# Kernel tuning notes

Hardware: AMD Instinct MI355X
Metric: run time of the kernel (lower is better)

## Reference

```python
import jax, jax.numpy as jnp
import numpy as np

B, S, D = 4, 4096, 64

def setup_inputs() -> dict:
    key = jax.random.key(0)
    kq, kk, kv, km = jax.random.split(key, 4)
    q = jax.random.normal(kq, (B, S, D), dtype=jnp.float32)
    k = jax.random.normal(kk, (B, S, D), dtype=jnp.float32)
    v = jax.random.normal(kv, (B, S, D), dtype=jnp.float32)
    # binary keep-mask in {0,1}; log(mask) -> {0, -inf}
    mask = (jax.random.uniform(km, (B, S)) > 0.2).astype(jnp.float32)
    return {"q": q, "k": k, "v": v, "mask": mask}

def reference(q, k, v, mask):
    emb_dim = q.shape[-1]
    qs = q / jnp.asarray(emb_dim, q.dtype) ** 0.5           # [B,S,D] scaled query
    scores = jnp.einsum('bqd,bkd->bqk', qs, k)              # [B,S,S]
    scores = scores + jnp.log(mask)[:, None, :]             # mask keys via log-add
    w = jax.nn.softmax(scores, axis=-1)                     # [B,S,S]
    out = jnp.einsum('bqk,bkd->bqd', w, v)                  # [B,S,D]
    # post-blend: masked query positions pass through the (scaled) query
    return out * mask[..., None] + qs * (1.0 - mask)[..., None]
```

## Files before the change

kernel.cpp:

```cpp
#include <hip/hip_runtime.h>
#include <hip/hip_bf16.h>

#define BATCH 4
#define SEQ   4096
#define DIM   64
#define TK    32

#if __has_builtin(__builtin_amdgcn_mfma_f32_16x16x16bf16_1k)
#define HAVE_1K 1
#else
#define HAVE_1K 0
#endif

typedef __attribute__((ext_vector_type(8))) short bf16x8;
typedef __attribute__((ext_vector_type(4))) short bf16x4;
typedef __attribute__((ext_vector_type(4))) float f32x4;

#define AS1 __attribute__((address_space(1)))
#define AS3 __attribute__((address_space(3)))

static __device__ __forceinline__ short f2bf(float x) {
    __hip_bfloat16 h = __float2bfloat16(x);
    return *reinterpret_cast<short*>(&h);
}
static __device__ __forceinline__ int pk2bf(float lo, float hi) {
    __hip_bfloat162 t = __float22bfloat162_rn(make_float2(lo, hi));
    int r; __builtin_memcpy(&r, &t, 4); return r;
}
static __device__ __forceinline__ bf16x4 mk4(const f32x4& s) {
    int2 t = make_int2(pk2bf(s[0], s[1]), pk2bf(s[2], s[3]));
    bf16x4 r; __builtin_memcpy(&r, &t, 8); return r;
}
static __device__ __forceinline__ void async16(const short* g, short* l) {
    __builtin_amdgcn_global_load_lds((const AS1 unsigned int*)g,
                                     (AS3 unsigned int*)l, 16, 0, 0);
}

__global__ __launch_bounds__(256)
void pack_kv(const float* __restrict__ kg, const float* __restrict__ vg,
             const float* __restrict__ mg,
             short* __restrict__ kp, short* __restrict__ vtp)
{
    if (blockIdx.x < 1024) {
        const int t   = blockIdx.x * 256 + threadIdx.x;
        const int row = t >> 4;
        const int d0  = (t & 15) * 4;
        f32x4 kv = *reinterpret_cast<const f32x4*>(kg + (size_t)row * DIM + d0);
        short4 ks;
        ks.x = f2bf(kv[0]); ks.y = f2bf(kv[1]); ks.z = f2bf(kv[2]); ks.w = f2bf(kv[3]);
        const int gs = (d0 >> 3) ^ (row & 7);
        *reinterpret_cast<short4*>(kp + (size_t)row * DIM + gs * 8 + (d0 & 7)) = ks;
    } else {
        __shared__ float Vl[64][66];
        __shared__ float Ml[64];
        const int t64 = blockIdx.x - 1024;
        const float* src = vg + (size_t)t64 * 64 * DIM;
        const int tid = threadIdx.x;
        #pragma unroll
        for (int i = 0; i < 4; ++i) {
            int idx = i * 256 + tid;
            int key = idx >> 4, part = idx & 15;
            f32x4 vv = *reinterpret_cast<const f32x4*>(src + (size_t)key * DIM + part * 4);
            float2* p0 = reinterpret_cast<float2*>(&Vl[key][part * 4]);
            p0[0] = make_float2(vv[0], vv[1]);
            p0[1] = make_float2(vv[2], vv[3]);
        }
        if (tid < 64) Ml[tid] = mg[(size_t)t64 * 64 + tid];
        __syncthreads();
        #pragma unroll
        for (int i = 0; i < 2; ++i) {
            const int gid = i * 256 + tid;
            const int t2 = gid >> 8;
            const int d  = (gid >> 2) & 63;
            const int g  = gid & 3;
            alignas(16) short s8[8];
            #pragma unroll
            for (int j = 0; j < 8; ++j) {
#if HAVE_1K
                const int key = t2 * 32 + (j >> 2) * 16 + g * 4 + (j & 3);
#else
                const int key = t2 * 32 + g * 8 + j;
#endif
                s8[j] = f2bf(Vl[key][d] * Ml[key]);
            }
            const int gs = g ^ ((d >> 1) & 3);
            short* dst = vtp + ((size_t)t64 * 2 + t2) * (TK * DIM) + d * TK + gs * 8;
            *reinterpret_cast<int4*>(dst) = *reinterpret_cast<const int4*>(s8);
        }
    }
}

template<int NSEG>
__global__ __launch_bounds__(256, 4)
void attn_fwd5(const float* __restrict__ qg, const float* __restrict__ mg,
               const short* __restrict__ kp, const short* __restrict__ vtp,
               float* __restrict__ outg, float* __restrict__ part)
{
    constexpr int SEGLEN = SEQ / NSEG;
    constexpr int ITERS  = SEGLEN / TK;

    __shared__ __align__(16) short Kl[2][TK][DIM];
    __shared__ __align__(16) short Vt[2][DIM][TK];

    const int tid  = threadIdx.x;
    const int wave = tid >> 6;
    const int lane = tid & 63;
    const int ln   = lane & 15;
    const int quad = lane >> 4;

    const int qblk = blockIdx.x & 31;
    const int rest = blockIdx.x >> 5;
    const int seg  = (NSEG == 1) ? 0 : (rest & (NSEG - 1));
    const int b    = (NSEG == 1) ? rest : (rest / NSEG);

    const int qw = qblk * 128 + wave * 32;
    const size_t bbase = (size_t)b * SEQ * DIM;

    const short* kb  = kp  + bbase + (size_t)seg * SEGLEN * DIM;
    const short* vb  = vtp + bbase + (size_t)seg * SEGLEN * DIM;
    const float* mgb = mg + (size_t)b * SEQ;

    const int gs0 = quad ^ (ln & 7);
    const int gsv = quad ^ ((ln >> 1) & 3);

#if !HAVE_1K
    const int idxA = ((lane & 16) * 2 + (lane & 15)) * 4;
    const int idxB = idxA + 64;
    const bool loquad = (quad < 2);
#endif

    bf16x8 aq[2][2];
    #pragma unroll
    for (int qt = 0; qt < 2; ++qt) {
        const float* qrow = qg + bbase + (size_t)(qw + qt * 16 + ln) * DIM;
        #pragma unroll
        for (int h = 0; h < 2; ++h) {
            alignas(16) short tmp[8];
            #pragma unroll
            for (int j = 0; j < 8; ++j)
                tmp[j] = f2bf(qrow[quad * 8 + h * 32 + j] * 0.125f);
            aq[qt][h] = *reinterpret_cast<bf16x8*>(tmp);
        }
    }

    f32x4 O[2][4];
    float lacc[2] = {0.f, 0.f};
    #pragma unroll
    for (int qt = 0; qt < 2; ++qt)
        #pragma unroll
        for (int i = 0; i < 4; ++i) O[qt][i] = (f32x4){0.f, 0.f, 0.f, 0.f};

    async16(kb + wave * 512 + lane * 8, &Kl[0][0][0] + wave * 512);
    async16(vb + wave * 512 + lane * 8, &Vt[0][0][0] + wave * 512);

    for (int t = 0; t < ITERS; ++t) {
        const int buf = t & 1;
        asm volatile("s_waitcnt vmcnt(0)" ::: "memory");
        __syncthreads();

        if (t + 1 < ITERS) {
            const short* gk = kb + (size_t)(t + 1) * TK * DIM;
            const short* gv = vb + (size_t)(t + 1) * TK * DIM;
            async16(gk + wave * 512 + lane * 8, &Kl[buf ^ 1][0][0] + wave * 512);
            async16(gv + wave * 512 + lane * 8, &Vt[buf ^ 1][0][0] + wave * 512);
        }

        const int key0 = seg * SEGLEN + t * TK;
        f32x4 m4[2];
        #pragma unroll
        for (int s = 0; s < 2; ++s)
            m4[s] = *reinterpret_cast<const f32x4*>(mgb + key0 + s * 16 + quad * 4);

        const short* klb = &Kl[buf][0][0];
        f32x4 sf[2][2];
        #pragma unroll
        for (int s = 0; s < 2; ++s) {
            bf16x8 ka0 = *reinterpret_cast<const bf16x8*>(klb + (s * 16 + ln) * DIM + gs0 * 8);
            bf16x8 ka1 = *reinterpret_cast<const bf16x8*>(klb + (s * 16 + ln) * DIM + (gs0 ^ 4) * 8);
            #pragma unroll
            for (int qt = 0; qt < 2; ++qt) {
                f32x4 acc = (f32x4){0.f, 0.f, 0.f, 0.f};
                acc = __builtin_amdgcn_mfma_f32_16x16x32_bf16(ka0, aq[qt][0], acc, 0, 0, 0);
                acc = __builtin_amdgcn_mfma_f32_16x16x32_bf16(ka1, aq[qt][1], acc, 0, 0, 0);
                sf[qt][s] = acc;
            }
        }

        #pragma unroll
        for (int qt = 0; qt < 2; ++qt)
            #pragma unroll
            for (int s = 0; s < 2; ++s)
                #pragma unroll
                for (int r = 0; r < 4; ++r) {
                    sf[qt][s][r] = __expf(sf[qt][s][r]);
                    lacc[qt] = fmaf(sf[qt][s][r], m4[s][r], lacc[qt]);
                }

        const short* vtb = &Vt[buf][0][0];
#if HAVE_1K
        bf16x4 bp[2][2];
        #pragma unroll
        for (int qt = 0; qt < 2; ++qt)
            #pragma unroll
            for (int s = 0; s < 2; ++s)
                bp[qt][s] = mk4(sf[qt][s]);
        #pragma unroll
        for (int ds = 0; ds < 4; ++ds) {
            bf16x8 vf = *reinterpret_cast<const bf16x8*>(vtb + (ds * 16 + ln) * TK + gsv * 8);
            bf16x4 va0 = __builtin_shufflevector(vf, vf, 0, 1, 2, 3);
            bf16x4 va1 = __builtin_shufflevector(vf, vf, 4, 5, 6, 7);
            #pragma unroll
            for (int qt = 0; qt < 2; ++qt) {
                O[qt][ds] = __builtin_amdgcn_mfma_f32_16x16x16bf16_1k(va0, bp[qt][0], O[qt][ds], 0, 0, 0);
                O[qt][ds] = __builtin_amdgcn_mfma_f32_16x16x16bf16_1k(va1, bp[qt][1], O[qt][ds], 0, 0, 0);
            }
        }
#else
        bf16x8 bfr[2];
        #pragma unroll
        for (int qt = 0; qt < 2; ++qt) {
            const int pk0_0 = pk2bf(sf[qt][0][0], sf[qt][0][1]);
            const int pk0_1 = pk2bf(sf[qt][0][2], sf[qt][0][3]);
            const int pk1_0 = pk2bf(sf[qt][1][0], sf[qt][1][1]);
            const int pk1_1 = pk2bf(sf[qt][1][2], sf[qt][1][3]);
            const int w0l = __builtin_amdgcn_ds_bpermute(idxA, pk0_0);
            const int w0h = __builtin_amdgcn_ds_bpermute(idxA, pk1_0);
            const int w1l = __builtin_amdgcn_ds_bpermute(idxA, pk0_1);
            const int w1h = __builtin_amdgcn_ds_bpermute(idxA, pk1_1);
            const int w2l = __builtin_amdgcn_ds_bpermute(idxB, pk0_0);
            const int w2h = __builtin_amdgcn_ds_bpermute(idxB, pk1_0);
            const int w3l = __builtin_amdgcn_ds_bpermute(idxB, pk0_1);
            const int w3h = __builtin_amdgcn_ds_bpermute(idxB, pk1_1);
            alignas(16) int bw[4];
            bw[0] = loquad ? w0l : w0h;
            bw[1] = loquad ? w1l : w1h;
            bw[2] = loquad ? w2l : w2h;
            bw[3] = loquad ? w3l : w3h;
            bfr[qt] = *reinterpret_cast<bf16x8*>(bw);
        }
        #pragma unroll
        for (int ds = 0; ds < 4; ++ds) {
            bf16x8 va = *reinterpret_cast<const bf16x8*>(vtb + (ds * 16 + ln) * TK + gsv * 8);
            #pragma unroll
            for (int qt = 0; qt < 2; ++qt)
                O[qt][ds] = __builtin_amdgcn_mfma_f32_16x16x32_bf16(va, bfr[qt], O[qt][ds], 0, 0, 0);
        }
#endif
    }

    #pragma unroll
    for (int qt = 0; qt < 2; ++qt) {
        lacc[qt] += __shfl_xor(lacc[qt], 16);
        lacc[qt] += __shfl_xor(lacc[qt], 32);
    }

    if (NSEG == 1) {
        #pragma unroll
        for (int qt = 0; qt < 2; ++qt) {
            const int qrow_i = qw + qt * 16 + ln;
            const float qm = mgb[qrow_i];
            const float inv = 1.0f / lacc[qt];
            const float* qrow = qg + bbase + (size_t)qrow_i * DIM;
            float* orow = outg + bbase + (size_t)qrow_i * DIM;
            #pragma unroll
            for (int ds = 0; ds < 4; ++ds) {
                const int d0 = ds * 16 + quad * 4;
                f32x4 o4;
                #pragma unroll
                for (int r = 0; r < 4; ++r) o4[r] = O[qt][ds][r] * inv;
                if (qm == 0.0f) {
                    f32x4 q4 = *reinterpret_cast<const f32x4*>(qrow + d0);
                    #pragma unroll
                    for (int r = 0; r < 4; ++r) o4[r] = q4[r] * 0.125f;
                }
                *reinterpret_cast<f32x4*>(orow + d0) = o4;
            }
        }
    } else {
        #pragma unroll
        for (int qt = 0; qt < 2; ++qt) {
            float* pb = part + (size_t)((b * SEQ + qw + qt * 16 + ln) * NSEG + seg) * 68;
            #pragma unroll
            for (int ds = 0; ds < 4; ++ds)
                *reinterpret_cast<f32x4*>(pb + ds * 16 + quad * 4) = O[qt][ds];
            if (quad == 0) pb[64] = lacc[qt];
        }
    }
}

template<int NSEG>
__global__ __launch_bounds__(256)
void combine_p(const float* __restrict__ part, const float* __restrict__ qg,
               const float* __restrict__ mg, float* __restrict__ outg)
{
    const int t = blockIdx.x * 256 + threadIdx.x;
    const int q = t >> 6;
    const int d = t & 63;
    const float* pb = part + (size_t)q * NSEG * 68;
    float acc = 0.f, den = 0.f;
    #pragma unroll
    for (int s = 0; s < NSEG; ++s) {
        acc += pb[s * 68 + d];
        den += pb[s * 68 + 64];
    }
    float out = acc / den;
    if (mg[q] == 0.0f) out = qg[t] * 0.125f;
    outg[t] = out;
}

extern "C" void kernel_launch(void* const* d_in, const int* in_sizes, int n_in,
                              void* d_out, int out_size, void* d_ws, size_t ws_size,
                              hipStream_t stream) {
    (void)in_sizes; (void)n_in; (void)out_size;
    const float* q = (const float*)d_in[0];
    const float* k = (const float*)d_in[1];
    const float* v = (const float*)d_in[2];
    const float* m = (const float*)d_in[3];
    float* out = (float*)d_out;

    const size_t nelem  = (size_t)BATCH * SEQ * DIM;
    const size_t packsz = nelem * 2 * sizeof(short);
    const size_t part8  = (size_t)BATCH * SEQ * 8 * 68 * sizeof(float);
    const size_t part4  = (size_t)BATCH * SEQ * 4 * 68 * sizeof(float);

    short* kp  = (short*)d_ws;
    short* vtp = kp + nelem;
    float* part = (float*)((char*)d_ws + packsz);

    pack_kv<<<dim3(1280), dim3(256), 0, stream>>>(k, v, m, kp, vtp);

    if (ws_size >= packsz + part8) {
        attn_fwd5<8><<<dim3(BATCH * 32 * 8), dim3(256), 0, stream>>>(q, m, kp, vtp, out, part);
        combine_p<8><<<dim3(BATCH * SEQ * DIM / 256), dim3(256), 0, stream>>>(part, q, m, out);
    } else if (ws_size >= packsz + part4) {
        attn_fwd5<4><<<dim3(BATCH * 32 * 4), dim3(256), 0, stream>>>(q, m, kp, vtp, out, part);
        combine_p<4><<<dim3(BATCH * SEQ * DIM / 256), dim3(256), 0, stream>>>(part, q, m, out);
    } else {
        attn_fwd5<1><<<dim3(BATCH * 32), dim3(256), 0, stream>>>(q, m, kp, vtp, out, nullptr);
    }
}
```

Baseline: 111.6 us.

## Double key tile to 64, use exp2 with folded log2e, repack V layout

```diff
diff --git a/kernel.cpp b/kernel.cpp
--- a/kernel.cpp
+++ b/kernel.cpp
@@ -4,7 +4,8 @@
 #define BATCH 4
 #define SEQ   4096
 #define DIM   64
-#define TK    32
+#define TK    64
+#define LOG2E 1.4426950408889634f
 
 #if __has_builtin(__builtin_amdgcn_mfma_f32_16x16x16bf16_1k)
 #define HAVE_1K 1
@@ -12,6 +13,12 @@
 #define HAVE_1K 0
 #endif
 
+#if __has_builtin(__builtin_amdgcn_exp2f)
+#define EXP2(x) __builtin_amdgcn_exp2f(x)
+#else
+#define EXP2(x) exp2f(x)
+#endif
+
 typedef __attribute__((ext_vector_type(8))) short bf16x8;
 typedef __attribute__((ext_vector_type(4))) short bf16x4;
 typedef __attribute__((ext_vector_type(4))) float f32x4;
@@ -30,6 +37,14 @@
 static __device__ __forceinline__ bf16x4 mk4(const f32x4& s) {
     int2 t = make_int2(pk2bf(s[0], s[1]), pk2bf(s[2], s[3]));
     bf16x4 r; __builtin_memcpy(&r, &t, 8); return r;
+}
+static __device__ __forceinline__ f32x4 mfma16(bf16x4 a, bf16x4 b, f32x4 c) {
+#if HAVE_1K
+    return __builtin_amdgcn_mfma_f32_16x16x16bf16_1k(a, b, c, 0, 0, 0);
+#else
+    asm("v_mfma_f32_16x16x16_bf16 %0, %1, %2, %0" : "+v"(c) : "v"(a), "v"(b));
+    return c;
+#endif
 }
 static __device__ __forceinline__ void async16(const short* g, short* l) {
     __builtin_amdgcn_global_load_lds((const AS1 unsigned int*)g,
@@ -41,20 +56,23 @@
              const float* __restrict__ mg,
              short* __restrict__ kp, short* __restrict__ vtp)
 {
-    if (blockIdx.x < 1024) {
-        const int t   = blockIdx.x * 256 + threadIdx.x;
-        const int row = t >> 4;
-        const int d0  = (t & 15) * 4;
-        f32x4 kv = *reinterpret_cast<const f32x4*>(kg + (size_t)row * DIM + d0);
-        short4 ks;
-        ks.x = f2bf(kv[0]); ks.y = f2bf(kv[1]); ks.z = f2bf(kv[2]); ks.w = f2bf(kv[3]);
-        const int gs = (d0 >> 3) ^ (row & 7);
-        *reinterpret_cast<short4*>(kp + (size_t)row * DIM + gs * 8 + (d0 & 7)) = ks;
+    if (blockIdx.x < 256) {
+        #pragma unroll
+        for (int i = 0; i < 4; ++i) {
+            const int unit = blockIdx.x * 1024 + i * 256 + threadIdx.x;
+            const int row = unit >> 4;
+            const int d0  = (unit & 15) * 4;
+            f32x4 kv = *reinterpret_cast<const f32x4*>(kg + (size_t)row * DIM + d0);
+            short4 ks;
+            ks.x = f2bf(kv[0]); ks.y = f2bf(kv[1]); ks.z = f2bf(kv[2]); ks.w = f2bf(kv[3]);
+            const int gs = (d0 >> 3) ^ (row & 7);
+            *reinterpret_cast<short4*>(kp + (size_t)row * DIM + gs * 8 + (d0 & 7)) = ks;
+        }
     } else {
         __shared__ float Vl[64][66];
         __shared__ float Ml[64];
-        const int t64 = blockIdx.x - 1024;
-        const float* src = vg + (size_t)t64 * 64 * DIM;
+        const int tile = blockIdx.x - 256;
+        const float* src = vg + (size_t)tile * TK * DIM;
         const int tid = threadIdx.x;
         #pragma unroll
         for (int i = 0; i < 4; ++i) {
@@ -65,26 +83,23 @@
             p0[0] = make_float2(vv[0], vv[1]);
             p0[1] = make_float2(vv[2], vv[3]);
         }
-        if (tid < 64) Ml[tid] = mg[(size_t)t64 * 64 + tid];
+        if (tid < 64) Ml[tid] = mg[(size_t)tile * TK + tid];
         __syncthreads();
         #pragma unroll
         for (int i = 0; i < 2; ++i) {
             const int gid = i * 256 + tid;
-            const int t2 = gid >> 8;
-            const int d  = (gid >> 2) & 63;
-            const int g  = gid & 3;
+            const int d = gid >> 3;
+            const int G = gid & 7;
+            const int qd = G >> 1, u = G & 1;
             alignas(16) short s8[8];
             #pragma unroll
-            for (int j = 0; j < 8; ++j) {
-#if HAVE_1K
-                const int key = t2 * 32 + (j >> 2) * 16 + g * 4 + (j & 3);
-#else
-                const int key = t2 * 32 + g * 8 + j;
-#endif
-                s8[j] = f2bf(Vl[key][d] * Ml[key]);
-            }
-            const int gs = g ^ ((d >> 1) & 3);
-            short* dst = vtp + ((size_t)t64 * 2 + t2) * (TK * DIM) + d * TK + gs * 8;
+            for (int e = 0; e < 8; ++e) {
+                const int v = e >> 2, j = e & 3;
+                const int key = (2 * u + v) * 16 + qd * 4 + j;
+                s8[e] = f2bf(Vl[key][d] * Ml[key]);
+            }
+            const int Gs = G ^ (d & 7);
+            short* dst = vtp + (size_t)tile * (TK * DIM) + d * TK + Gs * 8;
             *reinterpret_cast<int4*>(dst) = *reinterpret_cast<const int4*>(s8);
         }
     }
@@ -92,7 +107,7 @@
 
 template<int NSEG>
 __global__ __launch_bounds__(256, 4)
-void attn_fwd5(const float* __restrict__ qg, const float* __restrict__ mg,
+void attn_fwd6(const float* __restrict__ qg, const float* __restrict__ mg,
                const short* __restrict__ kp, const short* __restrict__ vtp,
                float* __restrict__ outg, float* __restrict__ part)
 {
@@ -121,13 +136,6 @@
     const float* mgb = mg + (size_t)b * SEQ;
 
     const int gs0 = quad ^ (ln & 7);
-    const int gsv = quad ^ ((ln >> 1) & 3);
-
-#if !HAVE_1K
-    const int idxA = ((lane & 16) * 2 + (lane & 15)) * 4;
-    const int idxB = idxA + 64;
-    const bool loquad = (quad < 2);
-#endif
 
     bf16x8 aq[2][2];
     #pragma unroll
@@ -138,7 +146,7 @@
             alignas(16) short tmp[8];
             #pragma unroll
             for (int j = 0; j < 8; ++j)
-                tmp[j] = f2bf(qrow[quad * 8 + h * 32 + j] * 0.125f);
+                tmp[j] = f2bf(qrow[quad * 8 + h * 32 + j] * (0.125f * LOG2E));
             aq[qt][h] = *reinterpret_cast<bf16x8*>(tmp);
         }
     }
@@ -150,8 +158,12 @@
         #pragma unroll
         for (int i = 0; i < 4; ++i) O[qt][i] = (f32x4){0.f, 0.f, 0.f, 0.f};
 
-    async16(kb + wave * 512 + lane * 8, &Kl[0][0][0] + wave * 512);
-    async16(vb + wave * 512 + lane * 8, &Vt[0][0][0] + wave * 512);
+    #pragma unroll
+    for (int i = 0; i < 2; ++i) {
+        const int c = wave * 2 + i;
+        async16(kb + c * 512 + lane * 8, &Kl[0][0][0] + c * 512);
+        async16(vb + c * 512 + lane * 8, &Vt[0][0][0] + c * 512);
+    }
 
     for (int t = 0; t < ITERS; ++t) {
         const int buf = t & 1;
@@ -161,91 +173,71 @@
         if (t + 1 < ITERS) {
             const short* gk = kb + (size_t)(t + 1) * TK * DIM;
             const short* gv = vb + (size_t)(t + 1) * TK * DIM;
-            async16(gk + wave * 512 + lane * 8, &Kl[buf ^ 1][0][0] + wave * 512);
-            async16(gv + wave * 512 + lane * 8, &Vt[buf ^ 1][0][0] + wave * 512);
+            #pragma unroll
+            for (int i = 0; i < 2; ++i) {
+                const int c = wave * 2 + i;
+                async16(gk + c * 512 + lane * 8, &Kl[buf ^ 1][0][0] + c * 512);
+                async16(gv + c * 512 + lane * 8, &Vt[buf ^ 1][0][0] + c * 512);
+            }
         }
 
         const int key0 = seg * SEGLEN + t * TK;
-        f32x4 m4[2];
-        #pragma unroll
-        for (int s = 0; s < 2; ++s)
-            m4[s] = *reinterpret_cast<const f32x4*>(mgb + key0 + s * 16 + quad * 4);
-
         const short* klb = &Kl[buf][0][0];
-        f32x4 sf[2][2];
-        #pragma unroll
-        for (int s = 0; s < 2; ++s) {
-            bf16x8 ka0 = *reinterpret_cast<const bf16x8*>(klb + (s * 16 + ln) * DIM + gs0 * 8);
-            bf16x8 ka1 = *reinterpret_cast<const bf16x8*>(klb + (s * 16 + ln) * DIM + (gs0 ^ 4) * 8);
+        const short* vtb = &Vt[buf][0][0];
+
+        #pragma unroll
+        for (int u = 0; u < 2; ++u) {
+            f32x4 m4[2];
+            #pragma unroll
+            for (int v = 0; v < 2; ++v)
+                m4[v] = *reinterpret_cast<const f32x4*>(
+                    mgb + key0 + (2 * u + v) * 16 + quad * 4);
+
+            f32x4 sf[2][2];
+            #pragma unroll
+            for (int v = 0; v < 2; ++v) {
+                const int s = 2 * u + v;
+                bf16x8 ka0 = *reinterpret_cast<const bf16x8*>(
+                    klb + (s * 16 + ln) * DIM + gs0 * 8);
+                bf16x8 ka1 = *reinterpret_cast<const bf16x8*>(
+                    klb + (s * 16 + ln) * DIM + (gs0 ^ 4) * 8);
+                #pragma unroll
+                for (int qt = 0; qt < 2; ++qt) {
+                    f32x4 acc = (f32x4){0.f, 0.f, 0.f, 0.f};
+                    acc = __builtin_amdgcn_mfma_f32_16x16x32_bf16(ka0, aq[qt][0], acc, 0, 0, 0);
+                    acc = __builtin_amdgcn_mfma_f32_16x16x32_bf16(ka1, aq[qt][1], acc, 0, 0, 0);
+                    sf[qt][v] = acc;
+                }
+            }
+
+            bf16x4 bp[2][2];
             #pragma unroll
             for (int qt = 0; qt < 2; ++qt) {
-                f32x4 acc = (f32x4){0.f, 0.f, 0.f, 0.f};
-                acc = __builtin_amdgcn_mfma_f32_16x16x32_bf16(ka0, aq[qt][0], acc, 0, 0, 0);
-                acc = __builtin_amdgcn_mfma_f32_16x16x32_bf16(ka1, aq[qt][1], acc, 0, 0, 0);
-                sf[qt][s] = acc;
-            }
-        }
-
-        #pragma unroll
-        for (int qt = 0; qt < 2; ++qt)
-            #pragma unroll
-            for (int s = 0; s < 2; ++s)
                 #pragma unroll
-                for (int r = 0; r < 4; ++r) {
-                    sf[qt][s][r] = __expf(sf[qt][s][r]);
-                    lacc[qt] = fmaf(sf[qt][s][r], m4[s][r], lacc[qt]);
+                for (int v = 0; v < 2; ++v) {
+                    #pragma unroll
+                    for (int r = 0; r < 4; ++r) {
+                        sf[qt][v][r] = EXP2(sf[qt][v][r]);
+                        lacc[qt] = fmaf(sf[qt][v][r], m4[v][r], lacc[qt]);
+                    }
+                    bp[qt][v] = mk4(sf[qt][v]);
                 }
-
-        const short* vtb = &Vt[buf][0][0];
-#if HAVE_1K
-        bf16x4 bp[2][2];
-        #pragma unroll
-        for (int qt = 0; qt < 2; ++qt)
-            #pragma unroll
-            for (int s = 0; s < 2; ++s)
-                bp[qt][s] = mk4(sf[qt][s]);
-        #pragma unroll
-        for (int ds = 0; ds < 4; ++ds) {
-            bf16x8 vf = *reinterpret_cast<const bf16x8*>(vtb + (ds * 16 + ln) * TK + gsv * 8);
-            bf16x4 va0 = __builtin_shufflevector(vf, vf, 0, 1, 2, 3);
-            bf16x4 va1 = __builtin_shufflevector(vf, vf, 4, 5, 6, 7);
-            #pragma unroll
-            for (int qt = 0; qt < 2; ++qt) {
-                O[qt][ds] = __builtin_amdgcn_mfma_f32_16x16x16bf16_1k(va0, bp[qt][0], O[qt][ds], 0, 0, 0);
-                O[qt][ds] = __builtin_amdgcn_mfma_f32_16x16x16bf16_1k(va1, bp[qt][1], O[qt][ds], 0, 0, 0);
-            }
-        }
-#else
-        bf16x8 bfr[2];
-        #pragma unroll
-        for (int qt = 0; qt < 2; ++qt) {
-            const int pk0_0 = pk2bf(sf[qt][0][0], sf[qt][0][1]);
-            const int pk0_1 = pk2bf(sf[qt][0][2], sf[qt][0][3]);
-            const int pk1_0 = pk2bf(sf[qt][1][0], sf[qt][1][1]);
-            const int pk1_1 = pk2bf(sf[qt][1][2], sf[qt][1][3]);
-            const int w0l = __builtin_amdgcn_ds_bpermute(idxA, pk0_0);
-            const int w0h = __builtin_amdgcn_ds_bpermute(idxA, pk1_0);
-            const int w1l = __builtin_amdgcn_ds_bpermute(idxA, pk0_1);
-            const int w1h = __builtin_amdgcn_ds_bpermute(idxA, pk1_1);
-            const int w2l = __builtin_amdgcn_ds_bpermute(idxB, pk0_0);
-            const int w2h = __builtin_amdgcn_ds_bpermute(idxB, pk1_0);
-            const int w3l = __builtin_amdgcn_ds_bpermute(idxB, pk0_1);
-            const int w3h = __builtin_amdgcn_ds_bpermute(idxB, pk1_1);
-            alignas(16) int bw[4];
-            bw[0] = loquad ? w0l : w0h;
-            bw[1] = loquad ? w1l : w1h;
-            bw[2] = loquad ? w2l : w2h;
-            bw[3] = loquad ? w3l : w3h;
-            bfr[qt] = *reinterpret_cast<bf16x8*>(bw);
-        }
-        #pragma unroll
-        for (int ds = 0; ds < 4; ++ds) {
-            bf16x8 va = *reinterpret_cast<const bf16x8*>(vtb + (ds * 16 + ln) * TK + gsv * 8);
-            #pragma unroll
-            for (int qt = 0; qt < 2; ++qt)
-                O[qt][ds] = __builtin_amdgcn_mfma_f32_16x16x32_bf16(va, bfr[qt], O[qt][ds], 0, 0, 0);
-        }
-#endif
+            }
+
+            const int gvu = (quad * 2 + u) ^ (ln & 7);
+            #pragma unroll
+            for (int ds = 0; ds < 4; ++ds) {
+                bf16x8 vf = *reinterpret_cast<const bf16x8*>(
+                    vtb + (ds * 16 + ln) * TK + gvu * 8);
+                bf16x4 va0 = __builtin_shufflevector(vf, vf, 0, 1, 2, 3);
+                bf16x4 va1 = __builtin_shufflevector(vf, vf, 4, 5, 6, 7);
+                #pragma unroll
+                for (int qt = 0; qt < 2; ++qt) {
+                    O[qt][ds] = mfma16(va0, bp[qt][0], O[qt][ds]);
+                    O[qt][ds] = mfma16(va1, bp[qt][1], O[qt][ds]);
+                }
+            }
+        }
     }
 
     #pragma unroll
@@ -327,15 +319,15 @@
     short* vtp = kp + nelem;
     float* part = (float*)((char*)d_ws + packsz);
 
-    pack_kv<<<dim3(1280), dim3(256), 0, stream>>>(k, v, m, kp, vtp);
+    pack_kv<<<dim3(512), dim3(256), 0, stream>>>(k, v, m, kp, vtp);
 
     if (ws_size >= packsz + part8) {
-        attn_fwd5<8><<<dim3(BATCH * 32 * 8), dim3(256), 0, stream>>>(q, m, kp, vtp, out, part);
+        attn_fwd6<8><<<dim3(BATCH * 32 * 8), dim3(256), 0, stream>>>(q, m, kp, vtp, out, part);
         combine_p<8><<<dim3(BATCH * SEQ * DIM / 256), dim3(256), 0, stream>>>(part, q, m, out);
     } else if (ws_size >= packsz + part4) {
-        attn_fwd5<4><<<dim3(BATCH * 32 * 4), dim3(256), 0, stream>>>(q, m, kp, vtp, out, part);
+        attn_fwd6<4><<<dim3(BATCH * 32 * 4), dim3(256), 0, stream>>>(q, m, kp, vtp, out, part);
         combine_p<4><<<dim3(BATCH * SEQ * DIM / 256), dim3(256), 0, stream>>>(part, q, m, out);
     } else {
-        attn_fwd5<1><<<dim3(BATCH * 32), dim3(256), 0, stream>>>(q, m, kp, vtp, out, nullptr);
-    }
-}
+        attn_fwd6<1><<<dim3(BATCH * 32), dim3(256), 0, stream>>>(q, m, kp, vtp, out, nullptr);
+    }
+}
```

Result: faster. 108.0 us (-3.3%).
